# Optimization experiments

Hardware: AMD Instinct MI355X
Metric: run time of the kernel (lower is better)

The kernel has to match this reference:

```python
import jax, jax.numpy as jnp
import numpy as np

N_NODES = 100000
N_EDGES = 1600000
HIDDEN = 128


def setup_inputs() -> dict:
    key = jax.random.key(0)
    ks = jax.random.split(key, 10)
    inp = {
        "hidden_states": jax.random.normal(ks[0], (N_NODES, HIDDEN), dtype=jnp.float32),
        "edges_i": jax.random.randint(ks[1], (2, N_EDGES), 0, N_NODES, dtype=jnp.int64),
        "edges_ii": jax.random.randint(ks[2], (2, N_EDGES), 0, N_NODES, dtype=jnp.int64),
        "edges_iii": jax.random.randint(ks[3], (2, N_EDGES), 0, N_NODES, dtype=jnp.int64),
        "edges_a": jax.random.randint(ks[4], (2, N_EDGES), 0, N_NODES, dtype=jnp.int64),
        # GCNConv weights (hidden -> hidden), no bias, Glorot-like init
        "W_i": jax.random.normal(ks[5], (HIDDEN, HIDDEN), dtype=jnp.float32) / np.sqrt(HIDDEN),
        "W_ii": jax.random.normal(ks[6], (HIDDEN, HIDDEN), dtype=jnp.float32) / np.sqrt(HIDDEN),
        "W_iii": jax.random.normal(ks[7], (HIDDEN, HIDDEN), dtype=jnp.float32) / np.sqrt(HIDDEN),
        "W_a": jax.random.normal(ks[8], (HIDDEN, HIDDEN), dtype=jnp.float32) / np.sqrt(HIDDEN),
    }
    return inp


def _gcn_conv(x, W, edges):
    # GCNConv with normalize=False, add_self_loops=False, bias=False:
    # out[dst] = sum over edges (x @ W)[src]
    xw = x @ W                                   # [N, H] small GEMM
    msg = jnp.take(xw, edges[0], axis=0)         # gather at src: [E, H]
    return jax.ops.segment_sum(msg, edges[1], num_segments=x.shape[0])


def reference(hidden_states, edges_i, edges_ii, edges_iii, edges_a, W_i, W_ii, W_iii, W_a):
    # VariationalNormalEpanechnikovDropout acts as identity in eval mode.
    x = hidden_states
    out = _gcn_conv(x, W_i, edges_i)
    out = out + _gcn_conv(x, W_ii, edges_ii)
    out = out + _gcn_conv(x, W_iii, edges_iii)
    out = out + _gcn_conv(x, W_a, edges_a)
    return out
```

## Files before the change

kernel.cpp:

```cpp
#include <hip/hip_runtime.h>


#define H 128
#define BSH 9
#define BNODES (1 << BSH)
#define SEGB (BNODES * 4)
#define EPB 16384

typedef __bf16 bf16x8 __attribute__((ext_vector_type(8)));
typedef float f32x4 __attribute__((ext_vector_type(4)));

static __device__ __forceinline__ ushort f2bf(float f) {
  union { float f; uint u; } v; v.f = f;
  uint r = (v.u + 0x7FFFu + ((v.u >> 16) & 1u)) >> 16;
  return (ushort)r;
}
static __device__ __forceinline__ float bflo(uint u) {
  union { uint u; float f; } v; v.u = u << 16; return v.f;
}
static __device__ __forceinline__ float bfhi(uint u) {
  union { uint u; float f; } v; v.u = u & 0xFFFF0000u; return v.f;
}

__global__ __launch_bounds__(256) void conv_prep(const float4* __restrict__ X4,
                                                 uint2* __restrict__ Xb2, int m,
                                                 const float* __restrict__ W0,
                                                 const float* __restrict__ W1,
                                                 const float* __restrict__ W2,
                                                 const float* __restrict__ W3,
                                                 ushort* __restrict__ Wt) {
  int i = blockIdx.x * 256 + threadIdx.x;
  if (i < m) {
    float4 v = X4[i];
    uint2 p;
    p.x = (uint)f2bf(v.x) | ((uint)f2bf(v.y) << 16);
    p.y = (uint)f2bf(v.z) | ((uint)f2bf(v.w) << 16);
    Xb2[i] = p;
  }
  if (i < 65536) {
    int kk = i & 127;
    int c = (i >> 7) & 127;
    int k = i >> 14;
    const float* W = (k == 0) ? W0 : (k == 1) ? W1 : (k == 2) ? W2 : W3;
    Wt[i] = f2bf(W[kk * 128 + c]);
  }
}

static __device__ __forceinline__ void fetch_edge(
    int gid, int c1, int c2, int c3,
    const int* d0, const int* d1, const int* d2, const int* d3,
    const int* s0, const int* s1, const int* s2, const int* s3,
    int& dst, int& src, int& k) {
  int i;
  const int *dp, *sp;
  if (gid < c1)      { k = 0; i = gid;      dp = d0; sp = s0; }
  else if (gid < c2) { k = 1; i = gid - c1; dp = d1; sp = s1; }
  else if (gid < c3) { k = 2; i = gid - c2; dp = d2; sp = s2; }
  else               { k = 3; i = gid - c3; dp = d3; sp = s3; }
  dst = dp[i];
  src = sp[i];
}

__global__ __launch_bounds__(256) void part_count(
    const int* __restrict__ d0, const int* __restrict__ d1,
    const int* __restrict__ d2, const int* __restrict__ d3,
    int c1, int c2, int c3, int tot, int nbin, int* __restrict__ hb) {
  __shared__ int lh[512];
  for (int i = threadIdx.x; i < nbin; i += 256) lh[i] = 0;
  __syncthreads();
  int base = blockIdx.x * EPB;
#pragma unroll 8
  for (int u = 0; u < EPB / 256; ++u) {
    int gid = base + u * 256 + threadIdx.x;
    if (gid < tot) {
      int i;
      const int* dp;
      if (gid < c1)      { i = gid;      dp = d0; }
      else if (gid < c2) { i = gid - c1; dp = d1; }
      else if (gid < c3) { i = gid - c2; dp = d2; }
      else               { i = gid - c3; dp = d3; }
      atomicAdd(&lh[dp[i] >> BSH], 1);
    }
  }
  __syncthreads();
  int* row = hb + (size_t)blockIdx.x * nbin;
  for (int i = threadIdx.x; i < nbin; i += 256) row[i] = lh[i];
}

__global__ __launch_bounds__(256) void part_scanA(int* __restrict__ hb,
                                                  int nblk, int nbin,
                                                  int* __restrict__ btot) {
  __shared__ int ws4[4];
  const int bin = blockIdx.x;
  const int t = threadIdx.x, lane = t & 63, wid = t >> 6;
  const int C = (nblk + 255) / 256;
  int b0 = t * C;
  int b1 = min(b0 + C, nblk);
  int s = 0;
  for (int b = b0; b < b1; ++b) s += hb[(size_t)b * nbin + bin];
  int incl = s;
#pragma unroll
  for (int d = 1; d < 64; d <<= 1) {
    int x = __shfl_up(incl, d, 64);
    if (lane >= d) incl += x;
  }
  if (lane == 63) ws4[wid] = incl;
  __syncthreads();
  if (t == 0) {
    int run = 0;
#pragma unroll
    for (int i = 0; i < 4; ++i) { int v = ws4[i]; ws4[i] = run; run += v; }
  }
  __syncthreads();
  int run = ws4[wid] + (incl - s);
  for (int b = b0; b < b1; ++b) {
    int v = hb[(size_t)b * nbin + bin];
    hb[(size_t)b * nbin + bin] = run;
    run += v;
  }
  if (t == 255) btot[bin] = run;
}

__global__ __launch_bounds__(512) void part_scanB(const int* __restrict__ btot,
                                                  int* __restrict__ binbase,
                                                  int nbin) {
  __shared__ int ws8[8];
  const int t = threadIdx.x, lane = t & 63, wid = t >> 6;
  int v = (t < nbin) ? btot[t] : 0;
  int incl = v;
#pragma unroll
  for (int d = 1; d < 64; d <<= 1) {
    int x = __shfl_up(incl, d, 64);
    if (lane >= d) incl += x;
  }
  if (lane == 63) ws8[wid] = incl;
  __syncthreads();
  if (t == 0) {
    int run = 0;
#pragma unroll
    for (int i = 0; i < 8; ++i) { int v2 = ws8[i]; ws8[i] = run; run += v2; }
  }
  __syncthreads();
  int excl = ws8[wid] + (incl - v);
  if (t < nbin) binbase[t] = excl;
  if (t == nbin - 1) binbase[nbin] = excl + v;
}

__global__ __launch_bounds__(256) void part_scatter(
    const int* __restrict__ d0, const int* __restrict__ d1,
    const int* __restrict__ d2, const int* __restrict__ d3,
    const int* __restrict__ s0, const int* __restrict__ s1,
    const int* __restrict__ s2, const int* __restrict__ s3,
    int c1, int c2, int c3, int tot, int nbin,
    const int* __restrict__ hb, const int* __restrict__ binbase,
    uint* __restrict__ part) {
  __shared__ int cur[512];
  const int* row = hb + (size_t)blockIdx.x * nbin;
  for (int i = threadIdx.x; i < nbin; i += 256) cur[i] = binbase[i] + row[i];
  __syncthreads();
  int base = blockIdx.x * EPB;
#pragma unroll 8
  for (int u = 0; u < EPB / 256; ++u) {
    int gid = base + u * 256 + threadIdx.x;
    if (gid < tot) {
      int dst, src, k;
      fetch_edge(gid, c1, c2, c3, d0, d1, d2, d3, s0, s1, s2, s3, dst, src, k);
      int pos = atomicAdd(&cur[dst >> BSH], 1);
      part[pos] = (uint)src | ((uint)(((dst & (BNODES - 1)) << 2) | k) << 17);
    }
  }
}

__global__ __launch_bounds__(1024) void build_bucket(
    const uint* __restrict__ part, const int* __restrict__ binbase,
    int* __restrict__ rp4, int* __restrict__ col_idx) {
  __shared__ int lh[SEGB];
  __shared__ int ws16[16];
  const int b = blockIdx.x;
  const int beg = binbase[b], end = binbase[b + 1];
  const int t = threadIdx.x, lane = t & 63, wid = t >> 6;

  lh[t] = 0;
  lh[t + 1024] = 0;
  __syncthreads();
  for (int i = beg + t; i < end; i += 1024)
    atomicAdd(&lh[part[i] >> 17], 1);
  __syncthreads();

  int v0 = lh[2 * t], v1 = lh[2 * t + 1];
  int s = v0 + v1;
  int incl = s;
#pragma unroll
  for (int d = 1; d < 64; d <<= 1) {
    int x = __shfl_up(incl, d, 64);
    if (lane >= d) incl += x;
  }
  if (lane == 63) ws16[wid] = incl;
  __syncthreads();
  if (t == 0) {
    int run = 0;
#pragma unroll
    for (int i = 0; i < 16; ++i) { int w = ws16[i]; ws16[i] = run; run += w; }
  }
  __syncthreads();
  int excl = beg + ws16[wid] + (incl - s);
  lh[2 * t] = excl;
  lh[2 * t + 1] = excl + v0;

  int gseg = b * SEGB + 2 * t;
  rp4[gseg] = excl;
  rp4[gseg + 1] = excl + v0;
  __syncthreads();

  for (int i = beg + t; i < end; i += 1024) {
    uint e = part[i];
    int pos = atomicAdd(&lh[e >> 17], 1);
    col_idx[pos] = (int)(e & 0x1FFFFu);
  }
}

#define ACC8(u)                                                       \
  do {                                                                \
    a0 += bflo((u).x); a1 += bfhi((u).x);                             \
    a2 += bflo((u).y); a3 += bfhi((u).y);                             \
    a4 += bflo((u).z); a5 += bfhi((u).z);                             \
    a6 += bflo((u).w); a7 += bfhi((u).w);                             \
  } while (0)

__global__ __launch_bounds__(256, 6) void gg(const uint* __restrict__ Xb,
                                             const int* __restrict__ rp4,
                                             const int* __restrict__ col_idx,
                                             const ushort* __restrict__ Wt,
                                             float* __restrict__ out, int n) {
  __shared__ uint sS[16][258];

  const int node0 = blockIdx.x * 16;
  const int wave = threadIdx.x >> 6;
  const int lane = threadIdx.x & 63;
  const int g = lane >> 4;
  const int qb = (lane & 15) * 4;

  int4 rpv[4];
  int rpE[4];
#pragma unroll
  for (int i = 0; i < 4; ++i) {
    int node = node0 + wave * 4 + i;
    rpv[i] = *(const int4*)(rp4 + (size_t)node * 4);
    rpE[i] = rp4[(size_t)node * 4 + 4];
  }
  int pe[4][4];
#pragma unroll
  for (int i = 0; i < 4; ++i) {
    pe[i][0] = (rpv[i].x + lane < rpv[i].y) ? col_idx[rpv[i].x + lane] : 0;
    pe[i][1] = (rpv[i].y + lane < rpv[i].z) ? col_idx[rpv[i].y + lane] : 0;
    pe[i][2] = (rpv[i].z + lane < rpv[i].w) ? col_idx[rpv[i].z + lane] : 0;
    pe[i][3] = (rpv[i].w + lane < rpE[i])   ? col_idx[rpv[i].w + lane] : 0;
  }

#pragma unroll
  for (int i = 0; i < 4; ++i) {
    int local = wave * 4 + i;
#pragma unroll
    for (int k = 0; k < 4; ++k) {
      int beg = (k == 0) ? rpv[i].x : (k == 1) ? rpv[i].y
              : (k == 2) ? rpv[i].z : rpv[i].w;
      int end = (k == 0) ? rpv[i].y : (k == 1) ? rpv[i].z
              : (k == 2) ? rpv[i].w : rpE[i];
      int p = pe[i][k];
      int len = end - beg;
      int m = (len > 64) ? 64 : len;
      float a0 = 0.f, a1 = 0.f, a2 = 0.f, a3 = 0.f;
      float a4 = 0.f, a5 = 0.f, a6 = 0.f, a7 = 0.f;
      int s = 0;
      for (; s + 8 <= m; s += 8) {
        int ea = __shfl(p, s + g, 64);
        int eb = __shfl(p, s + 4 + g, 64);
        uint4 ua = *(const uint4*)&Xb[(size_t)ea * 64 + qb];
        uint4 ub = *(const uint4*)&Xb[(size_t)eb * 64 + qb];
        ACC8(ua);
        ACC8(ub);
      }
      for (; s < m; s += 4) {
        int li = s + g;
        int e = __shfl(p, li, 64);
        if (li < m) {
          uint4 u = *(const uint4*)&Xb[(size_t)e * 64 + qb];
          ACC8(u);
        }
      }
      if (len > 64) {
        for (int j = beg + 64; j < end; j += 4) {
          int li = j + g;
          if (li < end) {
            int e = col_idx[li];
            uint4 u = *(const uint4*)&Xb[(size_t)e * 64 + qb];
            ACC8(u);
          }
        }
      }
      a0 += __shfl_xor(a0, 16, 64); a0 += __shfl_xor(a0, 32, 64);
      a1 += __shfl_xor(a1, 16, 64); a1 += __shfl_xor(a1, 32, 64);
      a2 += __shfl_xor(a2, 16, 64); a2 += __shfl_xor(a2, 32, 64);
      a3 += __shfl_xor(a3, 16, 64); a3 += __shfl_xor(a3, 32, 64);
      a4 += __shfl_xor(a4, 16, 64); a4 += __shfl_xor(a4, 32, 64);
      a5 += __shfl_xor(a5, 16, 64); a5 += __shfl_xor(a5, 32, 64);
      a6 += __shfl_xor(a6, 16, 64); a6 += __shfl_xor(a6, 32, 64);
      a7 += __shfl_xor(a7, 16, 64); a7 += __shfl_xor(a7, 32, 64);
      if (lane < 16) {
        uint* drow = &sS[local][k * 64 + qb];
        drow[0] = (uint)f2bf(a0) | ((uint)f2bf(a1) << 16);
        drow[1] = (uint)f2bf(a2) | ((uint)f2bf(a3) << 16);
        drow[2] = (uint)f2bf(a4) | ((uint)f2bf(a5) << 16);
        drow[3] = (uint)f2bf(a6) | ((uint)f2bf(a7) << 16);
      }
    }
  }
  __syncthreads();

  const ushort* sSu = (const ushort*)&sS[0][0];
  const int lr = lane & 15;
  const int lg = lane >> 4;
  const int cf0 = wave * 2;

  f32x4 acc0 = (f32x4)0.f, acc1 = (f32x4)0.f;

#pragma unroll
  for (int kc = 0; kc < 4; ++kc) {
#pragma unroll
    for (int k4 = 0; k4 < 4; ++k4) {
      bf16x8 a = *(const bf16x8*)&sSu[lr * 516 + kc * 128 + k4 * 32 + lg * 8];
      bf16x8 b0 = *(const bf16x8*)&Wt[kc * 16384 + (cf0 * 16 + lr) * 128 + k4 * 32 + lg * 8];
      bf16x8 b1 = *(const bf16x8*)&Wt[kc * 16384 + ((cf0 + 1) * 16 + lr) * 128 + k4 * 32 + lg * 8];
      acc0 = __builtin_amdgcn_mfma_f32_16x16x32_bf16(a, b0, acc0, 0, 0, 0);
      acc1 = __builtin_amdgcn_mfma_f32_16x16x32_bf16(a, b1, acc1, 0, 0, 0);
    }
  }

#pragma unroll
  for (int r = 0; r < 4; ++r) {
    int row = node0 + lg * 4 + r;
    if (row < n) {
      out[(size_t)row * H + cf0 * 16 + lr] = acc0[r];
      out[(size_t)row * H + (cf0 + 1) * 16 + lr] = acc1[r];
    }
  }
}

extern "C" void kernel_launch(void* const* d_in, const int* in_sizes, int n_in,
                              void* d_out, int out_size, void* d_ws, size_t ws_size,
                              hipStream_t stream) {
  const float* X = (const float*)d_in[0];
  const int* edges[4] = {(const int*)d_in[1], (const int*)d_in[2],
                         (const int*)d_in[3], (const int*)d_in[4]};
  const float* Wk[4] = {(const float*)d_in[5], (const float*)d_in[6],
                        (const float*)d_in[7], (const float*)d_in[8]};
  float* out = (float*)d_out;

  int n = in_sizes[0] / H;
  int nE[4];
  int tot = 0;
  for (int k = 0; k < 4; ++k) {
    nE[k] = in_sizes[1 + k] / 2;
    tot += nE[k];
  }
  int c1 = nE[0], c2 = c1 + nE[1], c3 = c2 + nE[2];
  int nbin = (n + BNODES - 1) >> BSH;
  int nblk = (tot + EPB - 1) / EPB;

  char* ws = (char*)d_ws;
  size_t off = 0;
  auto take = [&](size_t bytes) -> char* {
    char* p = ws + off;
    off = (off + bytes + 255) & ~(size_t)255;
    return p;
  };
  ushort* Wt = (ushort*)take(4 * 128 * 128 * sizeof(ushort));
  uint* Xb = (uint*)take((size_t)n * H * sizeof(ushort));
  int* hb = (int*)take((size_t)nblk * nbin * sizeof(int));
  int* btot = (int*)take((size_t)nbin * sizeof(int));
  int* binbase = (int*)take((size_t)(nbin + 1) * sizeof(int));
  int* rp4 = (int*)take(((size_t)nbin * SEGB + 1) * sizeof(int));
  uint* part = (uint*)take((size_t)tot * sizeof(uint));
  int* col_idx = (int*)take((size_t)tot * sizeof(int));

  const int* s0 = edges[0];
  const int* d0 = edges[0] + nE[0];
  const int* s1 = edges[1];
  const int* d1 = edges[1] + nE[1];
  const int* s2 = edges[2];
  const int* d2 = edges[2] + nE[2];
  const int* s3 = edges[3];
  const int* d3 = edges[3] + nE[3];

  conv_prep<<<(n * 32 + 255) / 256, 256, 0, stream>>>(
      (const float4*)X, (uint2*)Xb, n * 32, Wk[0], Wk[1], Wk[2], Wk[3], Wt);

  part_count<<<nblk, 256, 0, stream>>>(d0, d1, d2, d3, c1, c2, c3, tot, nbin, hb);
  part_scanA<<<nbin, 256, 0, stream>>>(hb, nblk, nbin, btot);
  part_scanB<<<1, 512, 0, stream>>>(btot, binbase, nbin);
  part_scatter<<<nblk, 256, 0, stream>>>(d0, d1, d2, d3, s0, s1, s2, s3,
                                         c1, c2, c3, tot, nbin, hb, binbase, part);
  build_bucket<<<nbin, 1024, 0, stream>>>(part, binbase, rp4, col_idx);

  gg<<<(n + 15) / 16, 256, 0, stream>>>(Xb, rp4, col_idx, Wt, out, n);
}
```

Before: 406.3 us.

## Fuse conversion with edge counting and merge scans via last-block ticket

Merges the bf16 conversion kernel and the destination-bin histogram kernel into one launch by giving them disjoint block ranges. The two scan kernels become one, using a global ticket counter so the last block to finish computes the bin bases. This cuts two kernel launches and their inter-kernel gaps. The gather kernel's occupancy hint is raised from 6 to 8 blocks per CU, which may add register pressure or spills. nbin is 196 here, so the final scan fits in one 256-thread block.

```diff
diff --git a/kernel.cpp b/kernel.cpp
--- a/kernel.cpp
+++ b/kernel.cpp
@@ -22,27 +22,114 @@
   union { uint u; float f; } v; v.u = u & 0xFFFF0000u; return v.f;
 }
 
-__global__ __launch_bounds__(256) void conv_prep(const float4* __restrict__ X4,
-                                                 uint2* __restrict__ Xb2, int m,
-                                                 const float* __restrict__ W0,
-                                                 const float* __restrict__ W1,
-                                                 const float* __restrict__ W2,
-                                                 const float* __restrict__ W3,
-                                                 ushort* __restrict__ Wt) {
-  int i = blockIdx.x * 256 + threadIdx.x;
-  if (i < m) {
-    float4 v = X4[i];
-    uint2 p;
-    p.x = (uint)f2bf(v.x) | ((uint)f2bf(v.y) << 16);
-    p.y = (uint)f2bf(v.z) | ((uint)f2bf(v.w) << 16);
-    Xb2[i] = p;
-  }
-  if (i < 65536) {
-    int kk = i & 127;
-    int c = (i >> 7) & 127;
-    int k = i >> 14;
-    const float* W = (k == 0) ? W0 : (k == 1) ? W1 : (k == 2) ? W2 : W3;
-    Wt[i] = f2bf(W[kk * 128 + c]);
+__global__ __launch_bounds__(256) void conv_count(
+    const float4* __restrict__ X4, uint2* __restrict__ Xb2, int m,
+    const float* __restrict__ W0, const float* __restrict__ W1,
+    const float* __restrict__ W2, const float* __restrict__ W3,
+    ushort* __restrict__ Wt,
+    const int* __restrict__ d0, const int* __restrict__ d1,
+    const int* __restrict__ d2, const int* __restrict__ d3,
+    int c1, int c2, int c3, int tot, int nbin, int nblk,
+    int* __restrict__ hb, int* __restrict__ ticket) {
+  __shared__ int lh[512];
+  if (blockIdx.x < nblk) {
+    if (blockIdx.x == 0 && threadIdx.x == 0) *ticket = 0;
+    for (int i = threadIdx.x; i < nbin; i += 256) lh[i] = 0;
+    __syncthreads();
+    int base = blockIdx.x * EPB;
+#pragma unroll 8
+    for (int u = 0; u < EPB / 256; ++u) {
+      int gid = base + u * 256 + threadIdx.x;
+      if (gid < tot) {
+        int i;
+        const int* dp;
+        if (gid < c1)      { i = gid;      dp = d0; }
+        else if (gid < c2) { i = gid - c1; dp = d1; }
+        else if (gid < c3) { i = gid - c2; dp = d2; }
+        else               { i = gid - c3; dp = d3; }
+        atomicAdd(&lh[dp[i] >> BSH], 1);
+      }
+    }
+    __syncthreads();
+    int* row = hb + (size_t)blockIdx.x * nbin;
+    for (int i = threadIdx.x; i < nbin; i += 256) row[i] = lh[i];
+  } else {
+    int i = (blockIdx.x - nblk) * 256 + threadIdx.x;
+    if (i < m) {
+      float4 v = X4[i];
+      uint2 p;
+      p.x = (uint)f2bf(v.x) | ((uint)f2bf(v.y) << 16);
+      p.y = (uint)f2bf(v.z) | ((uint)f2bf(v.w) << 16);
+      Xb2[i] = p;
+    }
+    if (i < 65536) {
+      int kk = i & 127;
+      int c = (i >> 7) & 127;
+      int k = i >> 14;
+      const float* W = (k == 0) ? W0 : (k == 1) ? W1 : (k == 2) ? W2 : W3;
+      Wt[i] = f2bf(W[kk * 128 + c]);
+    }
+  }
+}
+
+__global__ __launch_bounds__(256) void part_scan(
+    int* __restrict__ hb, int nblk, int nbin,
+    int* __restrict__ btot, int* __restrict__ binbase,
+    int* __restrict__ ticket) {
+  __shared__ int ws4[4];
+  __shared__ int isLast;
+  const int bin = blockIdx.x;
+  const int t = threadIdx.x, lane = t & 63, wid = t >> 6;
+  const int C = (nblk + 255) / 256;
+  int b0 = t * C;
+  int b1 = min(b0 + C, nblk);
+  int s = 0;
+  for (int b = b0; b < b1; ++b) s += hb[(size_t)b * nbin + bin];
+  int incl = s;
+#pragma unroll
+  for (int d = 1; d < 64; d <<= 1) {
+    int x = __shfl_up(incl, d, 64);
+    if (lane >= d) incl += x;
+  }
+  if (lane == 63) ws4[wid] = incl;
+  __syncthreads();
+  if (t == 0) {
+    int run = 0;
+#pragma unroll
+    for (int i = 0; i < 4; ++i) { int v = ws4[i]; ws4[i] = run; run += v; }
+  }
+  __syncthreads();
+  int run = ws4[wid] + (incl - s);
+  for (int b = b0; b < b1; ++b) {
+    int v = hb[(size_t)b * nbin + bin];
+    hb[(size_t)b * nbin + bin] = run;
+    run += v;
+  }
+  if (t == 255) atomicExch(&btot[bin], run);
+  __threadfence();
+  __syncthreads();
+  if (t == 0) isLast = (atomicAdd(ticket, 1) == (int)gridDim.x - 1);
+  __syncthreads();
+  if (isLast) {
+    int v = (t < nbin) ? atomicAdd(&btot[t], 0) : 0;
+    int incl2 = v;
+#pragma unroll
+    for (int d = 1; d < 64; d <<= 1) {
+      int x = __shfl_up(incl2, d, 64);
+      if (lane >= d) incl2 += x;
+    }
+    __syncthreads();
+    if (lane == 63) ws4[wid] = incl2;
+    __syncthreads();
+    if (t == 0) {
+      int run2 = 0;
+#pragma unroll
+      for (int i = 0; i < 4; ++i) { int v2 = ws4[i]; ws4[i] = run2; run2 += v2; }
+    }
+    __syncthreads();
+    int excl = ws4[wid] + (incl2 - v);
+    if (t < nbin) binbase[t] = excl;
+    if (t == nbin - 1) binbase[nbin] = excl + v;
   }
 }
 
@@ -61,91 +148,6 @@
   src = sp[i];
 }
 
-__global__ __launch_bounds__(256) void part_count(
-    const int* __restrict__ d0, const int* __restrict__ d1,
-    const int* __restrict__ d2, const int* __restrict__ d3,
-    int c1, int c2, int c3, int tot, int nbin, int* __restrict__ hb) {
-  __shared__ int lh[512];
-  for (int i = threadIdx.x; i < nbin; i += 256) lh[i] = 0;
-  __syncthreads();
-  int base = blockIdx.x * EPB;
-#pragma unroll 8
-  for (int u = 0; u < EPB / 256; ++u) {
-    int gid = base + u * 256 + threadIdx.x;
-    if (gid < tot) {
-      int i;
-      const int* dp;
-      if (gid < c1)      { i = gid;      dp = d0; }
-      else if (gid < c2) { i = gid - c1; dp = d1; }
-      else if (gid < c3) { i = gid - c2; dp = d2; }
-      else               { i = gid - c3; dp = d3; }
-      atomicAdd(&lh[dp[i] >> BSH], 1);
-    }
-  }
-  __syncthreads();
-  int* row = hb + (size_t)blockIdx.x * nbin;
-  for (int i = threadIdx.x; i < nbin; i += 256) row[i] = lh[i];
-}
-
-__global__ __launch_bounds__(256) void part_scanA(int* __restrict__ hb,
-                                                  int nblk, int nbin,
-                                                  int* __restrict__ btot) {
-  __shared__ int ws4[4];
-  const int bin = blockIdx.x;
-  const int t = threadIdx.x, lane = t & 63, wid = t >> 6;
-  const int C = (nblk + 255) / 256;
-  int b0 = t * C;
-  int b1 = min(b0 + C, nblk);
-  int s = 0;
-  for (int b = b0; b < b1; ++b) s += hb[(size_t)b * nbin + bin];
-  int incl = s;
-#pragma unroll
-  for (int d = 1; d < 64; d <<= 1) {
-    int x = __shfl_up(incl, d, 64);
-    if (lane >= d) incl += x;
-  }
-  if (lane == 63) ws4[wid] = incl;
-  __syncthreads();
-  if (t == 0) {
-    int run = 0;
-#pragma unroll
-    for (int i = 0; i < 4; ++i) { int v = ws4[i]; ws4[i] = run; run += v; }
-  }
-  __syncthreads();
-  int run = ws4[wid] + (incl - s);
-  for (int b = b0; b < b1; ++b) {
-    int v = hb[(size_t)b * nbin + bin];
-    hb[(size_t)b * nbin + bin] = run;
-    run += v;
-  }
-  if (t == 255) btot[bin] = run;
-}
-
-__global__ __launch_bounds__(512) void part_scanB(const int* __restrict__ btot,
-                                                  int* __restrict__ binbase,
-                                                  int nbin) {
-  __shared__ int ws8[8];
-  const int t = threadIdx.x, lane = t & 63, wid = t >> 6;
-  int v = (t < nbin) ? btot[t] : 0;
-  int incl = v;
-#pragma unroll
-  for (int d = 1; d < 64; d <<= 1) {
-    int x = __shfl_up(incl, d, 64);
-    if (lane >= d) incl += x;
-  }
-  if (lane == 63) ws8[wid] = incl;
-  __syncthreads();
-  if (t == 0) {
-    int run = 0;
-#pragma unroll
-    for (int i = 0; i < 8; ++i) { int v2 = ws8[i]; ws8[i] = run; run += v2; }
-  }
-  __syncthreads();
-  int excl = ws8[wid] + (incl - v);
-  if (t < nbin) binbase[t] = excl;
-  if (t == nbin - 1) binbase[nbin] = excl + v;
-}
-
 __global__ __launch_bounds__(256) void part_scatter(
     const int* __restrict__ d0, const int* __restrict__ d1,
     const int* __restrict__ d2, const int* __restrict__ d3,
@@ -227,7 +229,7 @@
     a6 += bflo((u).w); a7 += bfhi((u).w);                             \
   } while (0)
 
-__global__ __launch_bounds__(256, 6) void gg(const uint* __restrict__ Xb,
+__global__ __launch_bounds__(256, 8) void gg(const uint* __restrict__ Xb,
                                              const int* __restrict__ rp4,
                                              const int* __restrict__ col_idx,
                                              const ushort* __restrict__ Wt,
@@ -382,6 +384,7 @@
   int* rp4 = (int*)take(((size_t)nbin * SEGB + 1) * sizeof(int));
   uint* part = (uint*)take((size_t)tot * sizeof(uint));
   int* col_idx = (int*)take((size_t)tot * sizeof(int));
+  int* ticket = (int*)take(256);
 
   const int* s0 = edges[0];
   const int* d0 = edges[0] + nE[0];
@@ -392,12 +395,12 @@
   const int* s3 = edges[3];
   const int* d3 = edges[3] + nE[3];
 
-  conv_prep<<<(n * 32 + 255) / 256, 256, 0, stream>>>(
-      (const float4*)X, (uint2*)Xb, n * 32, Wk[0], Wk[1], Wk[2], Wk[3], Wt);
-
-  part_count<<<nblk, 256, 0, stream>>>(d0, d1, d2, d3, c1, c2, c3, tot, nbin, hb);
-  part_scanA<<<nbin, 256, 0, stream>>>(hb, nblk, nbin, btot);
-  part_scanB<<<1, 512, 0, stream>>>(btot, binbase, nbin);
+  int conv_blocks = (n * 32 + 255) / 256;
+  conv_count<<<nblk + conv_blocks, 256, 0, stream>>>(
+      (const float4*)X, (uint2*)Xb, n * 32, Wk[0], Wk[1], Wk[2], Wk[3], Wt,
+      d0, d1, d2, d3, c1, c2, c3, tot, nbin, nblk, hb, ticket);
+
+  part_scan<<<nbin, 256, 0, stream>>>(hb, nblk, nbin, btot, binbase, ticket);
   part_scatter<<<nblk, 256, 0, stream>>>(d0, d1, d2, d3, s0, s1, s2, s3,
                                          c1, c2, c3, tot, nbin, hb, binbase, part);
   build_bucket<<<nbin, 1024, 0, stream>>>(part, binbase, rp4, col_idx);
```

New measurement: 448.9 us. 10.5% more time.
